# Performance work log

Hardware: AMD Instinct MI355X
Metric: run time of the kernel (lower is better)

## Reference

```python
import jax, jax.numpy as jnp
import numpy as np


def pairwise_dist(x):
    # Euclidean cdist via the expansion trick; grad-safe sqrt (0 grad at 0, like torch).
    sq = jnp.sum(x * x, axis=1)
    d2 = sq[:, None] + sq[None, :] - 2.0 * (x @ x.T)
    d2 = jnp.maximum(d2, 0.0)
    pos = d2 > 0
    return jnp.where(pos, jnp.sqrt(jnp.where(pos, d2, 1.0)), 0.0)


def knn_mask(dist, k):
    # per-row ascending sort; skip index 0 (self), take next k neighbors
    idx = jnp.argsort(dist, axis=1)[:, 1:k + 1]            # [N, k]
    n = dist.shape[0]
    return jnp.zeros_like(dist).at[jnp.arange(n)[:, None], idx].set(1.0)


def setup_inputs() -> dict:
    key = jax.random.key(0)
    k1, k2 = jax.random.split(key)
    N, D, K = 8192, 64, 12
    latent = jax.random.normal(k1, (N, D), dtype=jnp.float32)
    latent_norm = jnp.ones((), dtype=jnp.float32)
    X = jax.random.normal(k2, (N, D), dtype=jnp.float32)
    dist_X = pairwise_dist(X)
    pair_mask_X = knn_mask(dist_X, K)
    return {"latent": latent, "latent_norm": latent_norm,
            "dist_X": dist_X, "pair_mask_X": pair_mask_X, "k": K}


def reference(latent, latent_norm, dist_X, pair_mask_X, k):
    n = latent.shape[0]
    dist_Z = pairwise_dist(latent) / latent_norm
    pair_mask_Z = knn_mask(dist_Z, k)

    mask_diff = pair_mask_Z - pair_mask_X
    matched = (n * k - jnp.sum(mask_diff != 0) * 0.5) / (n * k)

    # match_edges == 'symmetric'
    sig1 = dist_X * pair_mask_X
    sig1_2 = dist_Z * pair_mask_X
    distance1_2 = jnp.sum(jnp.square(sig1 - sig1_2))
    sig2 = dist_Z * pair_mask_Z
    sig2_1 = dist_X * pair_mask_Z
    distance2_1 = jnp.sum(jnp.square(sig2_1 - sig2))
    distance = distance1_2 + distance2_1
    return (distance, matched, distance1_2, distance2_1)
```

## Files before the change

### kernel.cpp

```cpp
#include <hip/hip_runtime.h>
#include <stdint.h>

constexpr int NPTS = 8192;
constexpr int DIM  = 64;
constexpr int KNN  = 12;

constexpr int RT = 64;
constexpr int CT = 64;
constexpr int CS = 8;
constexpr int STRIPE = NPTS / CS;
constexpr int NCHUNK = STRIPE / CT;
constexpr int LSTR = 72;
constexpr int CAP  = 28;
constexpr int BSTR = 29;

constexpr int NWG_DZ = (NPTS / RT) * CS;
constexpr int TOT4   = NPTS * NPTS / 4;
constexpr int WG4    = TOT4 / NWG_DZ;
constexpr int CH4    = WG4 / NCHUNK;

constexpr unsigned long long SENTINEL = 0xFFFFFFFFFFFFFFFFull;

typedef short bf16x8 __attribute__((ext_vector_type(8)));
typedef float f32x4  __attribute__((ext_vector_type(4)));

#define WG_BARRIER() asm volatile("s_waitcnt lgkmcnt(0)\n\ts_barrier" ::: "memory")

__device__ __forceinline__ unsigned short f2bf(float x) {
  unsigned u = __float_as_uint(x);
  return (unsigned short)((u + 0x7FFFu + ((u >> 16) & 1u)) >> 16);
}
__device__ __forceinline__ float bf2f(unsigned short h) {
  return __uint_as_float(((unsigned)h) << 16);
}

__global__ __launch_bounds__(256) void prep_kernel(
    const float* __restrict__ latent, unsigned short* __restrict__ Lh,
    unsigned short* __restrict__ Ll, float* __restrict__ sq,
    int* __restrict__ ecnt, float* __restrict__ out) {
  int i = blockIdx.x * 256 + threadIdx.x;
  ecnt[i] = 0;
  if (i < 4) out[i] = 0.0f;
  const float4* p = reinterpret_cast<const float4*>(latent + (size_t)i * DIM);
  float s = 0.f;
#pragma unroll
  for (int t = 0; t < DIM / 4; ++t) {
    float4 v = p[t];
    s += v.x * v.x + v.y * v.y + v.z * v.z + v.w * v.w;
    ushort4 h, l;
    h.x = f2bf(v.x); l.x = f2bf(v.x - bf2f(h.x));
    h.y = f2bf(v.y); l.y = f2bf(v.y - bf2f(h.y));
    h.z = f2bf(v.z); l.z = f2bf(v.z - bf2f(h.z));
    h.w = f2bf(v.w); l.w = f2bf(v.w - bf2f(h.w));
    *reinterpret_cast<ushort4*>(Lh + (size_t)i * DIM + t * 4) = h;
    *reinterpret_cast<ushort4*>(Ll + (size_t)i * DIM + t * 4) = l;
  }
  sq[i] = s;
}

__device__ __forceinline__ void topk_insert(unsigned long long cand,
                                            unsigned long long pk[KNN]) {
#pragma unroll
  for (int s = KNN - 1; s >= 0; --s) {
    bool belongs = cand < pk[s];
    bool shift = (s > 0) && (cand < pk[s - 1]);
    unsigned long long nv = shift ? pk[s - 1] : cand;
    if (belongs) pk[s] = nv;
  }
}

__device__ __forceinline__ void push_edge(int pos, int* __restrict__ ecnt,
                                          int* __restrict__ ecol) {
  int i = pos >> 13, j = pos & (NPTS - 1);
  int slot = atomicAdd(&ecnt[i], 1);
  if (slot < KNN) ecol[i * KNN + slot] = j;
}

__global__ __launch_bounds__(256, 3) void main_kernel(
    const unsigned short* __restrict__ Lh, const unsigned short* __restrict__ Ll,
    const float* __restrict__ sq, unsigned long long* __restrict__ topk_ws,
    const float* __restrict__ mask_X, int* __restrict__ ecnt,
    int* __restrict__ ecol) {
  __shared__ unsigned short Bh[2 * CT * LSTR], Bl[2 * CT * LSTR];
  __shared__ float d2b[RT * BSTR];
  __shared__ int   colb[RT * BSTR];
  __shared__ int   cnt[RT];
  __shared__ float thr[RT];
  __shared__ float sqA[RT];
  __shared__ float sqB[2][CT];
  __shared__ int   ovf;

  const int tid = threadIdx.x;
  const int tile = blockIdx.x / CS;
  const int split = blockIdx.x % CS;
  const int ib = tile * RT;
  const int jb0 = split * STRIPE;

  const int wid = tid >> 6;
  const int lane = tid & 63;
  const int quad = lane >> 4;
  const int l16 = lane & 15;
  const int wr = wid >> 1;
  const int wc = wid & 1;

  bf16x8 ahr[2][2], alr[2][2];
#pragma unroll
  for (int kk = 0; kk < 2; ++kk) {
    const int ko = kk * 32 + quad * 8;
#pragma unroll
    for (int rb = 0; rb < 2; ++rb) {
      const int row = ib + wr * 32 + rb * 16 + l16;
      ahr[kk][rb] = *reinterpret_cast<const bf16x8*>(Lh + (size_t)row * DIM + ko);
      alr[kk][rb] = *reinterpret_cast<const bf16x8*>(Ll + (size_t)row * DIM + ko);
    }
  }
  if (tid < RT) { sqA[tid] = sq[ib + tid]; thr[tid] = 3.4e38f; cnt[tid] = 0; }

  {
#pragma unroll
    for (int it = 0; it < 2; ++it) {
      int f = it * 256 + tid, r = f >> 3, c = f & 7;
      uint4 vh = *reinterpret_cast<const uint4*>(Lh + (size_t)(jb0 + r) * DIM + c * 8);
      uint4 vl = *reinterpret_cast<const uint4*>(Ll + (size_t)(jb0 + r) * DIM + c * 8);
      *reinterpret_cast<uint4*>(&Bh[r * LSTR + c * 8]) = vh;
      *reinterpret_cast<uint4*>(&Bl[r * LSTR + c * 8]) = vl;
    }
    if (tid < CT) sqB[0][tid] = sq[jb0 + tid];
  }
  __syncthreads();

  const f32x4* mbase = reinterpret_cast<const f32x4*>(mask_X);
  const int wgBase4 = blockIdx.x * WG4;

  unsigned long long pk[KNN];
#pragma unroll
  for (int t = 0; t < KNN; ++t) pk[t] = SENTINEL;

  for (int ch = 0; ch < NCHUNK; ++ch) {
    const int cur = ch & 1, nxt = cur ^ 1;
    const int jb = jb0 + ch * CT;
    const bool have_next = (ch + 1 < NCHUNK);

    uint4 vh0, vl0, vh1, vl1;
    float sqn = 0.f;
    if (have_next) {
      {
        int f = tid, r = f >> 3, c = f & 7;
        vh0 = *reinterpret_cast<const uint4*>(Lh + (size_t)(jb + CT + r) * DIM + c * 8);
        vl0 = *reinterpret_cast<const uint4*>(Ll + (size_t)(jb + CT + r) * DIM + c * 8);
      }
      {
        int f = 256 + tid, r = f >> 3, c = f & 7;
        vh1 = *reinterpret_cast<const uint4*>(Lh + (size_t)(jb + CT + r) * DIM + c * 8);
        vl1 = *reinterpret_cast<const uint4*>(Ll + (size_t)(jb + CT + r) * DIM + c * 8);
      }
      if (tid < CT) sqn = sq[jb + CT + tid];
    }
    f32x4 m[4];
    const int mb = wgBase4 + ch * CH4 + tid;
#pragma unroll
    for (int q = 0; q < 4; ++q)
      m[q] = __builtin_nontemporal_load(&mbase[mb + q * 256]);
    __builtin_amdgcn_sched_barrier(0);

    const int bbase = cur * CT * LSTR;
    f32x4 acc[2][2];
#pragma unroll
    for (int rb = 0; rb < 2; ++rb)
#pragma unroll
      for (int cb = 0; cb < 2; ++cb) acc[rb][cb] = (f32x4){0.f, 0.f, 0.f, 0.f};

#pragma unroll
    for (int kk = 0; kk < 2; ++kk) {
      const int ko = kk * 32 + quad * 8;
      bf16x8 bh[2], bl[2];
#pragma unroll
      for (int cb = 0; cb < 2; ++cb) {
        int col = wc * 32 + cb * 16 + l16;
        bh[cb] = *reinterpret_cast<const bf16x8*>(&Bh[bbase + col * LSTR + ko]);
        bl[cb] = *reinterpret_cast<const bf16x8*>(&Bl[bbase + col * LSTR + ko]);
      }
#pragma unroll
      for (int rb = 0; rb < 2; ++rb)
#pragma unroll
        for (int cb = 0; cb < 2; ++cb) {
          acc[rb][cb] = __builtin_amdgcn_mfma_f32_16x16x32_bf16(ahr[kk][rb], bh[cb], acc[rb][cb], 0, 0, 0);
          acc[rb][cb] = __builtin_amdgcn_mfma_f32_16x16x32_bf16(ahr[kk][rb], bl[cb], acc[rb][cb], 0, 0, 0);
          acc[rb][cb] = __builtin_amdgcn_mfma_f32_16x16x32_bf16(alr[kk][rb], bh[cb], acc[rb][cb], 0, 0, 0);
        }
    }

    unsigned todo = 0xFFFFu;
    int round = 0;
    do {
#pragma unroll
      for (int rb = 0; rb < 2; ++rb) {
#pragma unroll
        for (int r = 0; r < 4; ++r) {
          const int rl = wr * 32 + rb * 16 + quad * 4 + r;
          const int gi = ib + rl;
          const float sa = sqA[rl];
          const float tt = thr[rl];
#pragma unroll
          for (int cb = 0; cb < 2; ++cb) {
            const unsigned bit = 1u << (rb * 8 + r * 2 + cb);
            if (todo & bit) {
              const int col_l = wc * 32 + cb * 16 + l16;
              const int gj = jb + col_l;
              float d2 = sa + sqB[cur][col_l] - 2.0f * acc[rb][cb][r];
              float d2c = fmaxf(d2, 0.0f);
              if (d2c < tt && gj != gi) {
                int pos = atomicAdd(&cnt[rl], 1);
                if (pos < CAP) {
                  d2b[rl * BSTR + pos] = d2c;
                  colb[rl * BSTR + pos] = gj;
                  todo &= ~bit;
                }
              } else {
                todo &= ~bit;
              }
            }
          }
        }
      }
      if (round == 0 && have_next) {
        const int boff = nxt * CT * LSTR;
        { int f = tid, r = f >> 3, c = f & 7;
          *reinterpret_cast<uint4*>(&Bh[boff + r * LSTR + c * 8]) = vh0;
          *reinterpret_cast<uint4*>(&Bl[boff + r * LSTR + c * 8]) = vl0; }
        { int f = 256 + tid, r = f >> 3, c = f & 7;
          *reinterpret_cast<uint4*>(&Bh[boff + r * LSTR + c * 8]) = vh1;
          *reinterpret_cast<uint4*>(&Bl[boff + r * LSTR + c * 8]) = vl1; }
        if (tid < CT) sqB[nxt][tid] = sqn;
      }
      WG_BARRIER();

      if (tid < RT) {
        const int nraw = cnt[tid];
        const int n = nraw > CAP ? CAP : nraw;
        for (int t = 0; t < n; ++t) {
          unsigned long long cand =
              ((unsigned long long)__float_as_uint(d2b[tid * BSTR + t]) << 32) |
              (unsigned)colb[tid * BSTR + t];
          if (cand < pk[KNN - 1]) topk_insert(cand, pk);
        }
        thr[tid] = __uint_as_float((unsigned)(pk[KNN - 1] >> 32));
        cnt[tid] = 0;
        bool o = nraw > CAP;
        bool anyo = __any(o);
        if (tid == 0) ovf = anyo ? 1 : 0;
      }
      if (round == 0) {
#pragma unroll
        for (int q = 0; q < 4; ++q) {
          f32x4 mv = m[q];
          if (mv[0] == 0.f && mv[1] == 0.f && mv[2] == 0.f && mv[3] == 0.f) continue;
          const int base = (mb + q * 256) * 4;
          if (mv[0] != 0.f) push_edge(base + 0, ecnt, ecol);
          if (mv[1] != 0.f) push_edge(base + 1, ecnt, ecol);
          if (mv[2] != 0.f) push_edge(base + 2, ecnt, ecol);
          if (mv[3] != 0.f) push_edge(base + 3, ecnt, ecol);
        }
      }
      WG_BARRIER();
      ++round;
    } while (ovf != 0);
  }

  if (tid < RT) {
    size_t base = ((size_t)(ib + tid) * CS + split) * KNN;
#pragma unroll
    for (int t = 0; t < KNN; ++t) topk_ws[base + t] = pk[t];
  }
}

__global__ __launch_bounds__(256) void tail_kernel(
    const float* __restrict__ latent, const float* __restrict__ latent_norm,
    const float* __restrict__ dist_X, const int* __restrict__ ecol,
    const unsigned long long* __restrict__ topk_ws, float* __restrict__ d_out) {
  __shared__ float red[256];
  const int tid = threadIdx.x;
  const float invnorm = 1.0f / latent_norm[0];

  if (blockIdx.x < (NPTS * KNN / 256)) {
    const int e = blockIdx.x * 256 + tid;
    int i = e / KNN;
    int j = ecol[e];
    float dx = dist_X[(size_t)i * NPTS + j];
    const float4* a = reinterpret_cast<const float4*>(latent + (size_t)i * DIM);
    const float4* b = reinterpret_cast<const float4*>(latent + (size_t)j * DIM);
    float d2 = 0.f;
#pragma unroll
    for (int t = 0; t < DIM / 4; ++t) {
      float4 va = a[t], vb = b[t];
      float ex = va.x - vb.x, ey = va.y - vb.y, ez = va.z - vb.z, ew = va.w - vb.w;
      d2 += ex * ex + ey * ey + ez * ez + ew * ew;
    }
    float dz = (d2 > 0.f) ? sqrtf(d2) * invnorm : 0.f;
    float diff = dx - dz;

    red[tid] = diff * diff;
    __syncthreads();
    for (int s = 128; s > 0; s >>= 1) {
      if (tid < s) red[tid] += red[tid + s];
      __syncthreads();
    }
    if (tid == 0) {
      atomicAdd(&d_out[2], red[0]);
      atomicAdd(&d_out[0], red[0]);
    }
  } else {
    const int gi = (blockIdx.x - NPTS * KNN / 256) * 256 + tid;

    unsigned long long pk[KNN];
#pragma unroll
    for (int t = 0; t < KNN; ++t) pk[t] = SENTINEL;

    const unsigned long long* src = topk_ws + (size_t)gi * CS * KNN;
    for (int t = 0; t < CS * KNN; ++t) {
      unsigned long long cand = src[t];
      if (cand < pk[KNN - 1]) topk_insert(cand, pk);
    }

    int ec[KNN];
#pragma unroll
    for (int t = 0; t < KNN; ++t) ec[t] = ecol[gi * KNN + t];

    float acc2 = 0.f, accc = 0.f;
#pragma unroll
    for (int t = 0; t < KNN; ++t) {
      int j = (int)(unsigned)(pk[t] & 0xFFFFFFFFull);
      float d2 = __uint_as_float((unsigned)(pk[t] >> 32));
      float dz = (d2 > 0.0f) ? sqrtf(d2) * invnorm : 0.0f;
      float dxv = dist_X[(size_t)gi * NPTS + j];
      float diff = dxv - dz;
      acc2 += diff * diff;
      int hit = 0;
#pragma unroll
      for (int s = 0; s < KNN; ++s) hit |= (ec[s] == j);
      accc += (float)hit;
    }

    red[tid] = acc2;
    __syncthreads();
    for (int s = 128; s > 0; s >>= 1) {
      if (tid < s) red[tid] += red[tid + s];
      __syncthreads();
    }
    float racc2 = red[0];
    __syncthreads();
    red[tid] = accc;
    __syncthreads();
    for (int s = 128; s > 0; s >>= 1) {
      if (tid < s) red[tid] += red[tid + s];
      __syncthreads();
    }
    if (tid == 0) {
      atomicAdd(&d_out[3], racc2);
      atomicAdd(&d_out[0], racc2);
      atomicAdd(&d_out[1], red[0] * (1.0f / ((float)NPTS * (float)KNN)));
    }
  }
}

extern "C" void kernel_launch(void* const* d_in, const int* in_sizes, int n_in,
                              void* d_out, int out_size, void* d_ws,
                              size_t ws_size, hipStream_t stream) {
  const float* latent      = (const float*)d_in[0];
  const float* latent_norm = (const float*)d_in[1];
  const float* dist_X      = (const float*)d_in[2];
  const float* mask_X      = (const float*)d_in[3];
  float* out = (float*)d_out;

  char* w = (char*)d_ws;
  float*          sq   = (float*)w;                    w += NPTS * 4;
  unsigned short* Lh   = (unsigned short*)w;           w += NPTS * DIM * 2;
  unsigned short* Ll   = (unsigned short*)w;           w += NPTS * DIM * 2;
  int*            ecnt = (int*)w;                      w += NPTS * 4;
  int*            ecol = (int*)w;                      w += NPTS * KNN * 4;
  unsigned long long* topk = (unsigned long long*)w;

  prep_kernel<<<NPTS / 256, 256, 0, stream>>>(latent, Lh, Ll, sq, ecnt, out);
  main_kernel<<<NWG_DZ, 256, 0, stream>>>(Lh, Ll, sq, topk, mask_X, ecnt, ecol);
  tail_kernel<<<NPTS * KNN / 256 + NPTS / 256, 256, 0, stream>>>(
      latent, latent_norm, dist_X, ecol, topk, out);
}
```

Before: 707.4 us.

## Drop overflow retry loop, halve column splits, parallelize prep and gather dist_X in main

Removes the capped candidate buffer and its overflow-retry loop. The buffer stride grows to 65 so every candidate of a 64-column chunk fits, at the cost of more LDS and occupancy lowered to 2 workgroups. The column split drops from 8 to 4, giving fewer workgroups with longer stripes. prep now uses 8 threads per row with a shuffle reduction. dist_X values for X-mask edges are captured in main_kernel so the tail reads them contiguously. The tail's top-k merge runs one wavefront per block and uses shuffle reductions instead of LDS tree reductions.

```diff
diff --git a/kernel.cpp b/kernel.cpp
--- a/kernel.cpp
+++ b/kernel.cpp
@@ -7,12 +7,11 @@
 
 constexpr int RT = 64;
 constexpr int CT = 64;
-constexpr int CS = 8;
+constexpr int CS = 4;
 constexpr int STRIPE = NPTS / CS;
 constexpr int NCHUNK = STRIPE / CT;
 constexpr int LSTR = 72;
-constexpr int CAP  = 28;
-constexpr int BSTR = 29;
+constexpr int BSTR = 65;
 
 constexpr int NWG_DZ = (NPTS / RT) * CS;
 constexpr int TOT4   = NPTS * NPTS / 4;
@@ -38,24 +37,34 @@
     const float* __restrict__ latent, unsigned short* __restrict__ Lh,
     unsigned short* __restrict__ Ll, float* __restrict__ sq,
     int* __restrict__ ecnt, float* __restrict__ out) {
-  int i = blockIdx.x * 256 + threadIdx.x;
-  ecnt[i] = 0;
-  if (i < 4) out[i] = 0.0f;
-  const float4* p = reinterpret_cast<const float4*>(latent + (size_t)i * DIM);
-  float s = 0.f;
-#pragma unroll
-  for (int t = 0; t < DIM / 4; ++t) {
-    float4 v = p[t];
-    s += v.x * v.x + v.y * v.y + v.z * v.z + v.w * v.w;
-    ushort4 h, l;
-    h.x = f2bf(v.x); l.x = f2bf(v.x - bf2f(h.x));
-    h.y = f2bf(v.y); l.y = f2bf(v.y - bf2f(h.y));
-    h.z = f2bf(v.z); l.z = f2bf(v.z - bf2f(h.z));
-    h.w = f2bf(v.w); l.w = f2bf(v.w - bf2f(h.w));
-    *reinterpret_cast<ushort4*>(Lh + (size_t)i * DIM + t * 4) = h;
-    *reinterpret_cast<ushort4*>(Ll + (size_t)i * DIM + t * 4) = l;
-  }
-  sq[i] = s;
+  const int gid = blockIdx.x * 256 + threadIdx.x;
+  const int r = gid >> 3, o = gid & 7;
+  if (gid < 4) out[gid] = 0.0f;
+  if (o == 0) ecnt[r] = 0;
+
+  const float4* p = reinterpret_cast<const float4*>(latent + (size_t)r * DIM + o * 8);
+  float4 v0 = p[0], v1 = p[1];
+  float s = v0.x * v0.x + v0.y * v0.y + v0.z * v0.z + v0.w * v0.w +
+            v1.x * v1.x + v1.y * v1.y + v1.z * v1.z + v1.w * v1.w;
+
+  ushort4 h0, l0, h1, l1;
+  h0.x = f2bf(v0.x); l0.x = f2bf(v0.x - bf2f(h0.x));
+  h0.y = f2bf(v0.y); l0.y = f2bf(v0.y - bf2f(h0.y));
+  h0.z = f2bf(v0.z); l0.z = f2bf(v0.z - bf2f(h0.z));
+  h0.w = f2bf(v0.w); l0.w = f2bf(v0.w - bf2f(h0.w));
+  h1.x = f2bf(v1.x); l1.x = f2bf(v1.x - bf2f(h1.x));
+  h1.y = f2bf(v1.y); l1.y = f2bf(v1.y - bf2f(h1.y));
+  h1.z = f2bf(v1.z); l1.z = f2bf(v1.z - bf2f(h1.z));
+  h1.w = f2bf(v1.w); l1.w = f2bf(v1.w - bf2f(h1.w));
+  ushort4* dh = reinterpret_cast<ushort4*>(Lh + (size_t)r * DIM + o * 8);
+  ushort4* dl = reinterpret_cast<ushort4*>(Ll + (size_t)r * DIM + o * 8);
+  dh[0] = h0; dh[1] = h1;
+  dl[0] = l0; dl[1] = l1;
+
+  s += __shfl_xor(s, 1);
+  s += __shfl_xor(s, 2);
+  s += __shfl_xor(s, 4);
+  if (o == 0) sq[r] = s;
 }
 
 __device__ __forceinline__ void topk_insert(unsigned long long cand,
@@ -69,18 +78,23 @@
   }
 }
 
-__device__ __forceinline__ void push_edge(int pos, int* __restrict__ ecnt,
-                                          int* __restrict__ ecol) {
+__device__ __forceinline__ void push_edge(int pos, const float* __restrict__ dist_X,
+                                          int* __restrict__ ecnt,
+                                          int* __restrict__ ecol,
+                                          float* __restrict__ edx) {
   int i = pos >> 13, j = pos & (NPTS - 1);
   int slot = atomicAdd(&ecnt[i], 1);
-  if (slot < KNN) ecol[i * KNN + slot] = j;
-}
-
-__global__ __launch_bounds__(256, 3) void main_kernel(
+  if (slot < KNN) {
+    ecol[i * KNN + slot] = j;
+    edx[i * KNN + slot] = dist_X[pos];
+  }
+}
+
+__global__ __launch_bounds__(256, 2) void main_kernel(
     const unsigned short* __restrict__ Lh, const unsigned short* __restrict__ Ll,
     const float* __restrict__ sq, unsigned long long* __restrict__ topk_ws,
-    const float* __restrict__ mask_X, int* __restrict__ ecnt,
-    int* __restrict__ ecol) {
+    const float* __restrict__ mask_X, const float* __restrict__ dist_X,
+    int* __restrict__ ecnt, int* __restrict__ ecol, float* __restrict__ edx) {
   __shared__ unsigned short Bh[2 * CT * LSTR], Bl[2 * CT * LSTR];
   __shared__ float d2b[RT * BSTR];
   __shared__ int   colb[RT * BSTR];
@@ -88,7 +102,6 @@
   __shared__ float thr[RT];
   __shared__ float sqA[RT];
   __shared__ float sqB[2][CT];
-  __shared__ int   ovf;
 
   const int tid = threadIdx.x;
   const int tile = blockIdx.x / CS;
@@ -144,16 +157,12 @@
     uint4 vh0, vl0, vh1, vl1;
     float sqn = 0.f;
     if (have_next) {
-      {
-        int f = tid, r = f >> 3, c = f & 7;
+      { int f = tid, r = f >> 3, c = f & 7;
         vh0 = *reinterpret_cast<const uint4*>(Lh + (size_t)(jb + CT + r) * DIM + c * 8);
-        vl0 = *reinterpret_cast<const uint4*>(Ll + (size_t)(jb + CT + r) * DIM + c * 8);
-      }
-      {
-        int f = 256 + tid, r = f >> 3, c = f & 7;
+        vl0 = *reinterpret_cast<const uint4*>(Ll + (size_t)(jb + CT + r) * DIM + c * 8); }
+      { int f = 256 + tid, r = f >> 3, c = f & 7;
         vh1 = *reinterpret_cast<const uint4*>(Lh + (size_t)(jb + CT + r) * DIM + c * 8);
-        vl1 = *reinterpret_cast<const uint4*>(Ll + (size_t)(jb + CT + r) * DIM + c * 8);
-      }
+        vl1 = *reinterpret_cast<const uint4*>(Ll + (size_t)(jb + CT + r) * DIM + c * 8); }
       if (tid < CT) sqn = sq[jb + CT + tid];
     }
     f32x4 m[4];
@@ -190,81 +199,65 @@
         }
     }
 
-    unsigned todo = 0xFFFFu;
-    int round = 0;
-    do {
-#pragma unroll
-      for (int rb = 0; rb < 2; ++rb) {
-#pragma unroll
-        for (int r = 0; r < 4; ++r) {
-          const int rl = wr * 32 + rb * 16 + quad * 4 + r;
-          const int gi = ib + rl;
-          const float sa = sqA[rl];
-          const float tt = thr[rl];
-#pragma unroll
-          for (int cb = 0; cb < 2; ++cb) {
-            const unsigned bit = 1u << (rb * 8 + r * 2 + cb);
-            if (todo & bit) {
-              const int col_l = wc * 32 + cb * 16 + l16;
-              const int gj = jb + col_l;
-              float d2 = sa + sqB[cur][col_l] - 2.0f * acc[rb][cb][r];
-              float d2c = fmaxf(d2, 0.0f);
-              if (d2c < tt && gj != gi) {
-                int pos = atomicAdd(&cnt[rl], 1);
-                if (pos < CAP) {
-                  d2b[rl * BSTR + pos] = d2c;
-                  colb[rl * BSTR + pos] = gj;
-                  todo &= ~bit;
-                }
-              } else {
-                todo &= ~bit;
-              }
-            }
+#pragma unroll
+    for (int rb = 0; rb < 2; ++rb) {
+      const int row0 = wr * 32 + rb * 16 + quad * 4;
+#pragma unroll
+      for (int r = 0; r < 4; ++r) {
+        const int rl = row0 + r;
+        const int gi = ib + rl;
+        const float sa = sqA[rl];
+        const float tt = thr[rl];
+#pragma unroll
+        for (int cb = 0; cb < 2; ++cb) {
+          const int col_l = wc * 32 + cb * 16 + l16;
+          const int gj = jb + col_l;
+          float d2 = sa + sqB[cur][col_l] - 2.0f * acc[rb][cb][r];
+          float d2c = fmaxf(d2, 0.0f);
+          if (d2c < tt && gj != gi) {
+            int pos = atomicAdd(&cnt[rl], 1);
+            d2b[rl * BSTR + pos] = d2c;
+            colb[rl * BSTR + pos] = gj;
           }
         }
       }
-      if (round == 0 && have_next) {
-        const int boff = nxt * CT * LSTR;
-        { int f = tid, r = f >> 3, c = f & 7;
-          *reinterpret_cast<uint4*>(&Bh[boff + r * LSTR + c * 8]) = vh0;
-          *reinterpret_cast<uint4*>(&Bl[boff + r * LSTR + c * 8]) = vl0; }
-        { int f = 256 + tid, r = f >> 3, c = f & 7;
-          *reinterpret_cast<uint4*>(&Bh[boff + r * LSTR + c * 8]) = vh1;
-          *reinterpret_cast<uint4*>(&Bl[boff + r * LSTR + c * 8]) = vl1; }
-        if (tid < CT) sqB[nxt][tid] = sqn;
+    }
+
+    __builtin_amdgcn_sched_barrier(0);
+    if (have_next) {
+      const int boff = nxt * CT * LSTR;
+      { int f = tid, r = f >> 3, c = f & 7;
+        *reinterpret_cast<uint4*>(&Bh[boff + r * LSTR + c * 8]) = vh0;
+        *reinterpret_cast<uint4*>(&Bl[boff + r * LSTR + c * 8]) = vl0; }
+      { int f = 256 + tid, r = f >> 3, c = f & 7;
+        *reinterpret_cast<uint4*>(&Bh[boff + r * LSTR + c * 8]) = vh1;
+        *reinterpret_cast<uint4*>(&Bl[boff + r * LSTR + c * 8]) = vl1; }
+      if (tid < CT) sqB[nxt][tid] = sqn;
+    }
+    WG_BARRIER();
+
+    if (tid < RT) {
+      const int n = cnt[tid];
+      for (int t = 0; t < n; ++t) {
+        unsigned long long cand =
+            ((unsigned long long)__float_as_uint(d2b[tid * BSTR + t]) << 32) |
+            (unsigned)colb[tid * BSTR + t];
+        if (cand < pk[KNN - 1]) topk_insert(cand, pk);
       }
-      WG_BARRIER();
-
-      if (tid < RT) {
-        const int nraw = cnt[tid];
-        const int n = nraw > CAP ? CAP : nraw;
-        for (int t = 0; t < n; ++t) {
-          unsigned long long cand =
-              ((unsigned long long)__float_as_uint(d2b[tid * BSTR + t]) << 32) |
-              (unsigned)colb[tid * BSTR + t];
-          if (cand < pk[KNN - 1]) topk_insert(cand, pk);
-        }
-        thr[tid] = __uint_as_float((unsigned)(pk[KNN - 1] >> 32));
-        cnt[tid] = 0;
-        bool o = nraw > CAP;
-        bool anyo = __any(o);
-        if (tid == 0) ovf = anyo ? 1 : 0;
-      }
-      if (round == 0) {
-#pragma unroll
-        for (int q = 0; q < 4; ++q) {
-          f32x4 mv = m[q];
-          if (mv[0] == 0.f && mv[1] == 0.f && mv[2] == 0.f && mv[3] == 0.f) continue;
-          const int base = (mb + q * 256) * 4;
-          if (mv[0] != 0.f) push_edge(base + 0, ecnt, ecol);
-          if (mv[1] != 0.f) push_edge(base + 1, ecnt, ecol);
-          if (mv[2] != 0.f) push_edge(base + 2, ecnt, ecol);
-          if (mv[3] != 0.f) push_edge(base + 3, ecnt, ecol);
-        }
-      }
-      WG_BARRIER();
-      ++round;
-    } while (ovf != 0);
+      thr[tid] = __uint_as_float((unsigned)(pk[KNN - 1] >> 32));
+      cnt[tid] = 0;
+    }
+#pragma unroll
+    for (int q = 0; q < 4; ++q) {
+      f32x4 mv = m[q];
+      if (mv[0] == 0.f && mv[1] == 0.f && mv[2] == 0.f && mv[3] == 0.f) continue;
+      const int base = (mb + q * 256) * 4;
+      if (mv[0] != 0.f) push_edge(base + 0, dist_X, ecnt, ecol, edx);
+      if (mv[1] != 0.f) push_edge(base + 1, dist_X, ecnt, ecol, edx);
+      if (mv[2] != 0.f) push_edge(base + 2, dist_X, ecnt, ecol, edx);
+      if (mv[3] != 0.f) push_edge(base + 3, dist_X, ecnt, ecol, edx);
+    }
+    WG_BARRIER();
   }
 
   if (tid < RT) {
@@ -277,16 +270,17 @@
 __global__ __launch_bounds__(256) void tail_kernel(
     const float* __restrict__ latent, const float* __restrict__ latent_norm,
     const float* __restrict__ dist_X, const int* __restrict__ ecol,
-    const unsigned long long* __restrict__ topk_ws, float* __restrict__ d_out) {
-  __shared__ float red[256];
+    const float* __restrict__ edx, const unsigned long long* __restrict__ topk_ws,
+    float* __restrict__ d_out) {
   const int tid = threadIdx.x;
   const float invnorm = 1.0f / latent_norm[0];
 
   if (blockIdx.x < (NPTS * KNN / 256)) {
+    __shared__ float red[256];
     const int e = blockIdx.x * 256 + tid;
     int i = e / KNN;
     int j = ecol[e];
-    float dx = dist_X[(size_t)i * NPTS + j];
+    float dx = edx[e];
     const float4* a = reinterpret_cast<const float4*>(latent + (size_t)i * DIM);
     const float4* b = reinterpret_cast<const float4*>(latent + (size_t)j * DIM);
     float d2 = 0.f;
@@ -310,7 +304,8 @@
       atomicAdd(&d_out[0], red[0]);
     }
   } else {
-    const int gi = (blockIdx.x - NPTS * KNN / 256) * 256 + tid;
+    if (tid >= 64) return;
+    const int gi = (blockIdx.x - NPTS * KNN / 256) * 64 + tid;
 
     unsigned long long pk[KNN];
 #pragma unroll
@@ -341,24 +336,15 @@
       accc += (float)hit;
     }
 
-    red[tid] = acc2;
-    __syncthreads();
-    for (int s = 128; s > 0; s >>= 1) {
-      if (tid < s) red[tid] += red[tid + s];
-      __syncthreads();
-    }
-    float racc2 = red[0];
-    __syncthreads();
-    red[tid] = accc;
-    __syncthreads();
-    for (int s = 128; s > 0; s >>= 1) {
-      if (tid < s) red[tid] += red[tid + s];
-      __syncthreads();
+#pragma unroll
+    for (int s = 32; s > 0; s >>= 1) {
+      acc2 += __shfl_down(acc2, s);
+      accc += __shfl_down(accc, s);
     }
     if (tid == 0) {
-      atomicAdd(&d_out[3], racc2);
-      atomicAdd(&d_out[0], racc2);
-      atomicAdd(&d_out[1], red[0] * (1.0f / ((float)NPTS * (float)KNN)));
+      atomicAdd(&d_out[3], acc2);
+      atomicAdd(&d_out[0], acc2);
+      atomicAdd(&d_out[1], accc * (1.0f / ((float)NPTS * (float)KNN)));
     }
   }
 }
@@ -378,10 +364,12 @@
   unsigned short* Ll   = (unsigned short*)w;           w += NPTS * DIM * 2;
   int*            ecnt = (int*)w;                      w += NPTS * 4;
   int*            ecol = (int*)w;                      w += NPTS * KNN * 4;
+  float*          edx  = (float*)w;                    w += NPTS * KNN * 4;
   unsigned long long* topk = (unsigned long long*)w;
 
-  prep_kernel<<<NPTS / 256, 256, 0, stream>>>(latent, Lh, Ll, sq, ecnt, out);
-  main_kernel<<<NWG_DZ, 256, 0, stream>>>(Lh, Ll, sq, topk, mask_X, ecnt, ecol);
-  tail_kernel<<<NPTS * KNN / 256 + NPTS / 256, 256, 0, stream>>>(
-      latent, latent_norm, dist_X, ecol, topk, out);
-}
+  prep_kernel<<<NPTS * 8 / 256, 256, 0, stream>>>(latent, Lh, Ll, sq, ecnt, out);
+  main_kernel<<<NWG_DZ, 256, 0, stream>>>(Lh, Ll, sq, topk, mask_X, dist_X,
+                                          ecnt, ecol, edx);
+  tail_kernel<<<NPTS * KNN / 256 + NPTS / 64, 256, 0, stream>>>(
+      latent, latent_norm, dist_X, ecol, edx, topk, out);
+}
```

Result: faster. 617.0 us (-12.8%).
